# Performance work log

Hardware: AMD Instinct MI355X
Metric: run time of the kernel (lower is better)

Reference implementation:

```python
import jax, jax.numpy as jnp
import numpy as np

N_EMBD = 4096
N_HEAD = 2
HEAD_DIM = N_EMBD // N_HEAD  # 2048; note seq_len T must equal HEAD_DIM for the bias broadcast
B, T = 8, HEAD_DIM


def setup_inputs() -> dict:
    key = jax.random.key(0)
    ks = jax.random.split(key, 6)
    s = 1.0 / np.sqrt(N_EMBD)
    return {
        "x": jax.random.normal(ks[0], (B, T, N_EMBD), dtype=jnp.float32),
        "Wq": jax.random.normal(ks[1], (N_EMBD, N_EMBD), dtype=jnp.float32) * s,
        "Wk": jax.random.normal(ks[2], (N_EMBD, N_EMBD), dtype=jnp.float32) * s,
        "Wv": jax.random.normal(ks[3], (N_EMBD, N_EMBD), dtype=jnp.float32) * s,
        "Wo": jax.random.normal(ks[4], (N_EMBD, N_EMBD), dtype=jnp.float32) * s,
        "position_bias": jax.random.normal(ks[5], (N_HEAD, HEAD_DIM), dtype=jnp.float32) * 0.02,
    }


def reference(x, Wq, Wk, Wv, Wo, position_bias):
    Bb, Tt, C = x.shape
    H, D = N_HEAD, C // N_HEAD
    # nn.Linear(bias=False): y = x @ W.T
    q = (x @ Wq.T).reshape(Bb, Tt, H, D).transpose(0, 2, 1, 3)  # (B,H,T,D)
    k = (x @ Wk.T).reshape(Bb, Tt, H, D).transpose(0, 2, 1, 3)
    v = (x @ Wv.T).reshape(Bb, Tt, H, D).transpose(0, 2, 1, 3)
    scale = 1.0 / jnp.sqrt(jnp.asarray(D, dtype=x.dtype))
    scores = jnp.einsum("bhtd,bhsd->bhts", q, k) * scale  # (B,H,T,T)
    # position_bias (H,D) -> (1,H,1,D); broadcasts over key axis since D == T
    scores = scores + position_bias[None, :, None, :]
    atten = jax.nn.softmax(scores, axis=-1)  # mask=None, dropout=0.0 -> identity
    y = jnp.einsum("bhts,bhsd->bhtd", atten, v)  # (B,H,T,D)
    y = y.transpose(0, 2, 1, 3).reshape(Bb, Tt, C)
    y = y @ Wo.T
    return (y, atten)
```

## Files before the change

### kernel.cpp

```cpp
#include <hip/hip_runtime.h>
#include <hip/hip_bf16.h>
#include <cstdint>
#include <cstddef>


typedef short short8_t __attribute__((ext_vector_type(8)));
typedef float f32x4   __attribute__((ext_vector_type(4)));

__device__ __forceinline__ short f2bf(float f) {
  unsigned u = __builtin_bit_cast(unsigned, f);
  u = (u + 0x7FFFu + ((u >> 16) & 1u)) >> 16;
  return (short)u;
}

__device__ __forceinline__ short8_t cvt8(float4 a, float4 b) {
  short8_t r;
  r[0] = f2bf(a.x); r[1] = f2bf(a.y); r[2] = f2bf(a.z); r[3] = f2bf(a.w);
  r[4] = f2bf(b.x); r[5] = f2bf(b.y); r[6] = f2bf(b.z); r[7] = f2bf(b.w);
  return r;
}

__device__ __forceinline__ void gld_lds16(const void* g, void* l) {
  __builtin_amdgcn_global_load_lds(
      (const __attribute__((address_space(1))) void*)g,
      (__attribute__((address_space(3))) void*)l, 16, 0, 0);
}

__global__ __launch_bounds__(256)
void cvt_f32_bf16(const float* __restrict__ src, short* __restrict__ dst, int n8) {
  for (int i = blockIdx.x * blockDim.x + threadIdx.x; i < n8;
       i += gridDim.x * blockDim.x) {
    const float4* p = (const float4*)(src + (size_t)i * 8);
    float4 a = p[0], b = p[1];
    *(short8_t*)(dst + (size_t)i * 8) = cvt8(a, b);
  }
}

template<int MODE>
__global__ __launch_bounds__(512, 2)
void gemm256(const short* __restrict__ Ag, const short* __restrict__ Bg,
             void* __restrict__ Cg, const float* __restrict__ bias) {
  constexpr int K  = (MODE == 3 || MODE == 4) ? 2048 : 4096;
  constexpr int NS = K / 32;

  __shared__ short lds[65536];

  const int tid = threadIdx.x;

  const int bid = blockIdx.x;
  const int id  = (bid & 7) * (gridDim.x >> 3) + (bid >> 3);

  int m0, n0, z = 0;
  size_t aoff = 0, boff = 0;
  if constexpr (MODE == 3 || MODE == 4) {
    z  = id >> 6;
    m0 = ((id >> 3) & 7) << 8;
    n0 = (id & 7) << 8;
    aoff = boff = (size_t)z << 22;
  } else {
    m0 = (id >> 4) << 8;
    n0 = (id & 15) << 8;
  }

  const int r0 = tid >> 2;
  const int qs = ((tid & 3) ^ ((r0 >> 1) & 3)) << 3;
  const short* Ap0 = Ag + aoff + (size_t)(m0 + r0) * K + qs;
  const short* Ap1 = Ap0 + (size_t)128 * K;
  const short* Bp0 = Bg + boff + (size_t)(n0 + r0) * K + qs;
  const short* Bp1 = Bp0 + (size_t)128 * K;
  short* la0 = &lds[0]    + tid * 8;
  short* la1 = la0 + 4096;
  short* lb0 = &lds[8192] + tid * 8;
  short* lb1 = lb0 + 4096;

  auto STAGE = [&](int t) {
    const int s = (t & 3) * 16384;
    const int k = t * 32;
    gld_lds16(Ap0 + k, la0 + s);
    gld_lds16(Ap1 + k, la1 + s);
    gld_lds16(Bp0 + k, lb0 + s);
    gld_lds16(Bp1 + k, lb1 + s);
  };

  const int l  = tid & 63;
  const int fr = l & 15;
  const int kq = l >> 4;
  const int wm = (tid >> 8) << 7;
  const int wn = ((tid >> 6) & 3) << 6;
  const int slotP = (kq ^ ((fr >> 1) & 3)) << 3;
  const int aB = (wm + fr) * 32 + slotP;
  const int bB = 8192 + (wn + fr) * 32 + slotP;

  f32x4 acc[8][4] = {};

  STAGE(0); STAGE(1); STAGE(2);

  for (int p = 0; p < NS; ++p) {
    if (p + 3 < NS) {
      STAGE(p + 3);
      asm volatile("s_waitcnt vmcnt(12)" ::: "memory");
    } else if (p + 2 < NS) {
      asm volatile("s_waitcnt vmcnt(8)" ::: "memory");
    } else if (p + 1 < NS) {
      asm volatile("s_waitcnt vmcnt(4)" ::: "memory");
    } else {
      asm volatile("s_waitcnt vmcnt(0)" ::: "memory");
    }
    __builtin_amdgcn_s_barrier();
    __builtin_amdgcn_sched_barrier(0);

    const short* sl = &lds[(p & 3) * 16384];
    short8_t af[8], bf[4];
#pragma unroll
    for (int m = 0; m < 8; ++m) af[m] = *(const short8_t*)&sl[aB + m * 512];
#pragma unroll
    for (int n = 0; n < 4; ++n) bf[n] = *(const short8_t*)&sl[bB + n * 512];
    __builtin_amdgcn_s_setprio(1);
#pragma unroll
    for (int m = 0; m < 8; ++m)
#pragma unroll
      for (int n = 0; n < 4; ++n)
        acc[m][n] = __builtin_amdgcn_mfma_f32_16x16x32_bf16(af[m], bf[n], acc[m][n], 0, 0, 0);
    __builtin_amdgcn_s_setprio(0);
    __builtin_amdgcn_sched_barrier(0);
    __builtin_amdgcn_s_barrier();
  }

#pragma unroll
  for (int m = 0; m < 8; ++m) {
#pragma unroll
    for (int n = 0; n < 4; ++n) {
#pragma unroll
      for (int r = 0; r < 4; ++r) {
        const int gm = m0 + wm + m * 16 + kq * 4 + r;
        const int gn = n0 + wn + n * 16 + fr;
        const float v = acc[m][n][r];
        if constexpr (MODE == 0) {
          short* dst = (short*)Cg;
          const int bh = ((gm >> 11) << 1) + (gn >> 11);
          dst[((size_t)bh << 22) + ((size_t)(gm & 2047) << 11) + (gn & 2047)] = f2bf(v);
        } else if constexpr (MODE == 2) {
          short* dst = (short*)Cg;
          const int bh = ((gm >> 11) << 1) + (gn >> 11);
          dst[((size_t)bh << 22) + ((size_t)(gn & 2047) << 11) + (gm & 2047)] = f2bf(v);
        } else if constexpr (MODE == 3) {
          float* dst = (float*)Cg;
          const float sv = v * 0.022097086912079608f + bias[((z & 1) << 11) + gn];
          dst[((size_t)z << 22) + ((size_t)gm << 11) + gn] = sv;
        } else if constexpr (MODE == 4) {
          short* dst = (short*)Cg;
          const size_t row = ((size_t)(z >> 1) << 11) + gm;
          dst[(row << 12) + ((size_t)(z & 1) << 11) + gn] = f2bf(v);
        } else {
          float* dst = (float*)Cg;
          dst[(size_t)gm * 4096 + gn] = v;
        }
      }
    }
  }
}

__global__ __launch_bounds__(256)
void softmax_rows(float* __restrict__ attn, short* __restrict__ outb) {
  float* row  = attn + ((size_t)blockIdx.x << 11);
  short* rowb = outb + ((size_t)blockIdx.x << 11);
  const int tid = threadIdx.x;

  float4 v0 = *(const float4*)(row + tid * 8);
  float4 v1 = *(const float4*)(row + tid * 8 + 4);

  float m = fmaxf(fmaxf(fmaxf(v0.x, v0.y), fmaxf(v0.z, v0.w)),
                  fmaxf(fmaxf(v1.x, v1.y), fmaxf(v1.z, v1.w)));
#pragma unroll
  for (int off = 1; off < 64; off <<= 1) m = fmaxf(m, __shfl_xor(m, off));

  __shared__ float redm[4];
  __shared__ float reds[4];
  if ((tid & 63) == 0) redm[tid >> 6] = m;
  __syncthreads();
  m = fmaxf(fmaxf(redm[0], redm[1]), fmaxf(redm[2], redm[3]));

  float e[8];
  e[0] = expf(v0.x - m); e[1] = expf(v0.y - m); e[2] = expf(v0.z - m); e[3] = expf(v0.w - m);
  e[4] = expf(v1.x - m); e[5] = expf(v1.y - m); e[6] = expf(v1.z - m); e[7] = expf(v1.w - m);
  float s = 0.f;
#pragma unroll
  for (int i = 0; i < 8; ++i) s += e[i];
#pragma unroll
  for (int off = 1; off < 64; off <<= 1) s += __shfl_xor(s, off);
  if ((tid & 63) == 0) reds[tid >> 6] = s;
  __syncthreads();
  s = reds[0] + reds[1] + reds[2] + reds[3];

  const float inv = 1.0f / s;
  float4 o0, o1;
  o0.x = e[0] * inv; o0.y = e[1] * inv; o0.z = e[2] * inv; o0.w = e[3] * inv;
  o1.x = e[4] * inv; o1.y = e[5] * inv; o1.z = e[6] * inv; o1.w = e[7] * inv;
  *(float4*)(row + tid * 8)     = o0;
  *(float4*)(row + tid * 8 + 4) = o1;
  *(short8_t*)(rowb + tid * 8)  = cvt8(o0, o1);
}

extern "C" void kernel_launch(void* const* d_in, const int* in_sizes, int n_in,
                              void* d_out, int out_size, void* d_ws, size_t ws_size,
                              hipStream_t stream) {
  const float* x  = (const float*)d_in[0];
  const float* Wq = (const float*)d_in[1];
  const float* Wk = (const float*)d_in[2];
  const float* Wv = (const float*)d_in[3];
  const float* Wo = (const float*)d_in[4];
  const float* pb = (const float*)d_in[5];

  float* y_out = (float*)d_out;
  float* attn  = y_out + (size_t)8 * 2048 * 4096;

  const size_t NEED = 4ull * 67108864ull * 2ull;
  if (ws_size < NEED) return;
  short* buf0 = (short*)d_ws;
  short* buf1 = buf0 + 67108864;
  short* buf2 = buf1 + 67108864;
  short* buf3 = buf2 + 67108864;

  short* xb      = buf0;
  short* qb      = buf1;
  short* kb      = buf2;
  short* vtb     = buf3;
  short* wob     = buf0;
  short* attn_bf = buf1;
  short* yb      = buf2;
  short* wb      = (short*)attn;

  const dim3 blk512(512);
  const dim3 blk(256);
  const dim3 gcv(2048);
  const dim3 g1k(1024);

  cvt_f32_bf16<<<gcv, blk, 0, stream>>>(x, xb, 67108864 / 8);

  cvt_f32_bf16<<<gcv, blk, 0, stream>>>(Wq, wb, 16777216 / 8);
  gemm256<0><<<g1k, blk512, 0, stream>>>(xb, wb, qb, nullptr);
  cvt_f32_bf16<<<gcv, blk, 0, stream>>>(Wk, wb, 16777216 / 8);
  gemm256<0><<<g1k, blk512, 0, stream>>>(xb, wb, kb, nullptr);
  cvt_f32_bf16<<<gcv, blk, 0, stream>>>(Wv, wb, 16777216 / 8);
  gemm256<2><<<g1k, blk512, 0, stream>>>(xb, wb, vtb, nullptr);

  cvt_f32_bf16<<<gcv, blk, 0, stream>>>(Wo, wob, 16777216 / 8);

  gemm256<3><<<g1k, blk512, 0, stream>>>(qb, kb, attn, pb);
  softmax_rows<<<dim3(32768), blk, 0, stream>>>(attn, attn_bf);
  gemm256<4><<<g1k, blk512, 0, stream>>>(attn_bf, vtb, yb, nullptr);
  gemm256<5><<<g1k, blk512, 0, stream>>>(yb, wob, y_out, nullptr);
}
```

Measured before the change: 3.011 ms.

## Double-buffer MFMA register fragments to prefetch next LDS stage during compute

Restructures the GEMM main loop so that the fragments for stage p+1 are read from LDS into a second register set while the MFMAs for stage p run, using a ping-pong pair of fragment arrays and a two-phase unrolled loop. Wait counts shift by one stage, and the sched_barriers that kept the LDS reads separate from the MFMA block are removed so the compiler can interleave them. The goal is to hide LDS read latency behind matrix math. In exchange it holds twelve more short8 fragments in registers, which raises register pressure under the 512-thread, 2-block launch bound and risks spills.

```diff
diff --git a/kernel.cpp b/kernel.cpp
--- a/kernel.cpp
+++ b/kernel.cpp
@@ -92,38 +92,50 @@
   const int bB = 8192 + (wn + fr) * 32 + slotP;
 
   f32x4 acc[8][4] = {};
-
-  STAGE(0); STAGE(1); STAGE(2);
-
-  for (int p = 0; p < NS; ++p) {
+  short8_t fA[8], fB[4], gA[8], gB[4];
+
+  auto phase = [&](int p, short8_t (&cA)[8], short8_t (&cB)[4],
+                   short8_t (&nA)[8], short8_t (&nB)[4]) {
     if (p + 3 < NS) {
       STAGE(p + 3);
-      asm volatile("s_waitcnt vmcnt(12)" ::: "memory");
+      asm volatile("s_waitcnt vmcnt(8)" ::: "memory");
     } else if (p + 2 < NS) {
-      asm volatile("s_waitcnt vmcnt(8)" ::: "memory");
+      asm volatile("s_waitcnt vmcnt(4)" ::: "memory");
     } else if (p + 1 < NS) {
-      asm volatile("s_waitcnt vmcnt(4)" ::: "memory");
-    } else {
       asm volatile("s_waitcnt vmcnt(0)" ::: "memory");
     }
     __builtin_amdgcn_s_barrier();
-    __builtin_amdgcn_sched_barrier(0);
-
-    const short* sl = &lds[(p & 3) * 16384];
-    short8_t af[8], bf[4];
-#pragma unroll
-    for (int m = 0; m < 8; ++m) af[m] = *(const short8_t*)&sl[aB + m * 512];
-#pragma unroll
-    for (int n = 0; n < 4; ++n) bf[n] = *(const short8_t*)&sl[bB + n * 512];
+    if (p + 1 < NS) {
+      const short* sl = &lds[((p + 1) & 3) * 16384];
+#pragma unroll
+      for (int m = 0; m < 8; ++m) nA[m] = *(const short8_t*)&sl[aB + m * 512];
+#pragma unroll
+      for (int n = 0; n < 4; ++n) nB[n] = *(const short8_t*)&sl[bB + n * 512];
+    }
     __builtin_amdgcn_s_setprio(1);
 #pragma unroll
     for (int m = 0; m < 8; ++m)
 #pragma unroll
       for (int n = 0; n < 4; ++n)
-        acc[m][n] = __builtin_amdgcn_mfma_f32_16x16x32_bf16(af[m], bf[n], acc[m][n], 0, 0, 0);
+        acc[m][n] = __builtin_amdgcn_mfma_f32_16x16x32_bf16(cA[m], cB[n], acc[m][n], 0, 0, 0);
     __builtin_amdgcn_s_setprio(0);
-    __builtin_amdgcn_sched_barrier(0);
     __builtin_amdgcn_s_barrier();
+  };
+
+  STAGE(0); STAGE(1); STAGE(2);
+  asm volatile("s_waitcnt vmcnt(8)" ::: "memory");
+  __builtin_amdgcn_s_barrier();
+  {
+    const short* sl = &lds[0];
+#pragma unroll
+    for (int m = 0; m < 8; ++m) fA[m] = *(const short8_t*)&sl[aB + m * 512];
+#pragma unroll
+    for (int n = 0; n < 4; ++n) fB[n] = *(const short8_t*)&sl[bB + n * 512];
+  }
+
+  for (int p = 0; p < NS; p += 2) {
+    phase(p,     fA, fB, gA, gB);
+    phase(p + 1, gA, gB, fA, fB);
   }
 
 #pragma unroll
```

Result: faster. 2.925 ms (-2.9%).

## Split GEMM k-step into two half-phases with fragment-ordered LDS layout

Applied to the files above, without the earlier changes.

Reworks the GEMM mainloop so each 32-wide k-step runs in two halves. Each half issues half of the next stage's global-to-LDS loads and loads A fragments for half of the M tiles, with barriers between halves so memory traffic interleaves with MFMA work. The LDS tile layout changes from a swizzled row-major layout to a per-16-row fragment-contiguous layout, so each lane reads one contiguous 16-byte chunk without XOR swizzling. This adds barriers per iteration and changes the vmcnt accounting, which risks extra sync stalls or ordering mistakes.

```diff
diff --git a/kernel.cpp b/kernel.cpp
--- a/kernel.cpp
+++ b/kernel.cpp
@@ -62,70 +62,94 @@
     n0 = (id & 15) << 8;
   }
 
-  const int r0 = tid >> 2;
-  const int qs = ((tid & 3) ^ ((r0 >> 1) & 3)) << 3;
-  const short* Ap0 = Ag + aoff + (size_t)(m0 + r0) * K + qs;
-  const short* Ap1 = Ap0 + (size_t)128 * K;
-  const short* Bp0 = Bg + boff + (size_t)(n0 + r0) * K + qs;
-  const short* Bp1 = Bp0 + (size_t)128 * K;
-  short* la0 = &lds[0]    + tid * 8;
-  short* la1 = la0 + 4096;
-  short* lb0 = &lds[8192] + tid * 8;
-  short* lb1 = lb0 + 4096;
-
-  auto STAGE = [&](int t) {
-    const int s = (t & 3) * 16384;
+  const int l = tid & 63;
+  const int w = tid >> 6;
+
+  const int srow = l & 15;
+  const int skol = (l >> 4) * 8;
+  const short* ApS  = Ag + aoff + (size_t)(m0 + 2 * w * 16 + srow) * K + skol;
+  const short* ApS2 = ApS + (size_t)16 * K;
+  const short* BpS  = Bg + boff + (size_t)(n0 + 2 * w * 16 + srow) * K + skol;
+  const short* BpS2 = BpS + (size_t)16 * K;
+
+  auto STAGE0 = [&](int t) {
+    const int s = (t & 3) << 14;
     const int k = t * 32;
-    gld_lds16(Ap0 + k, la0 + s);
-    gld_lds16(Ap1 + k, la1 + s);
-    gld_lds16(Bp0 + k, lb0 + s);
-    gld_lds16(Bp1 + k, lb1 + s);
+    gld_lds16(ApS + k, &lds[s + 2 * w * 512]);
+    gld_lds16(BpS + k, &lds[s + 8192 + 2 * w * 512]);
   };
-
-  const int l  = tid & 63;
+  auto STAGE1 = [&](int t) {
+    const int s = (t & 3) << 14;
+    const int k = t * 32;
+    gld_lds16(ApS2 + k, &lds[s + (2 * w + 1) * 512]);
+    gld_lds16(BpS2 + k, &lds[s + 8192 + (2 * w + 1) * 512]);
+  };
+
+  const int wmF = (tid >> 8) * 8;
+  const int wnF = ((tid >> 6) & 3) * 4;
+  const int l8  = l * 8;
+
+  f32x4 acc[8][4] = {};
+
+  STAGE0(0); STAGE1(0); STAGE0(1); STAGE1(1); STAGE0(2); STAGE1(2);
+  asm volatile("s_waitcnt vmcnt(8)" ::: "memory");
+  __builtin_amdgcn_s_barrier();
+
+  for (int p = 0; p < NS; ++p) {
+    const int slot = (p & 3) << 14;
+    short8_t A4[4], B4[4], A8[4];
+
+#pragma unroll
+    for (int n = 0; n < 4; ++n)
+      B4[n] = *(const short8_t*)&lds[slot + 8192 + (wnF + n) * 512 + l8];
+#pragma unroll
+    for (int i = 0; i < 4; ++i)
+      A4[i] = *(const short8_t*)&lds[slot + (wmF + i) * 512 + l8];
+    if (p + 3 < NS) STAGE0(p + 3);
+    __builtin_amdgcn_sched_barrier(0);
+    __builtin_amdgcn_s_barrier();
+    asm volatile("s_waitcnt lgkmcnt(0)" ::: "memory");
+    __builtin_amdgcn_sched_barrier(0);
+    __builtin_amdgcn_s_setprio(1);
+#pragma unroll
+    for (int i = 0; i < 4; ++i)
+#pragma unroll
+      for (int n = 0; n < 4; ++n)
+        acc[i][n] = __builtin_amdgcn_mfma_f32_16x16x32_bf16(A4[i], B4[n], acc[i][n], 0, 0, 0);
+    __builtin_amdgcn_s_setprio(0);
+    __builtin_amdgcn_sched_barrier(0);
+    __builtin_amdgcn_s_barrier();
+
+#pragma unroll
+    for (int i = 0; i < 4; ++i)
+      A8[i] = *(const short8_t*)&lds[slot + (wmF + 4 + i) * 512 + l8];
+    if (p + 3 < NS) {
+      STAGE1(p + 3);
+      asm volatile("s_waitcnt vmcnt(8)" ::: "memory");
+    } else if (p + 2 < NS) {
+      asm volatile("s_waitcnt vmcnt(4)" ::: "memory");
+    } else if (p + 1 < NS) {
+      asm volatile("s_waitcnt vmcnt(0)" ::: "memory");
+    }
+    __builtin_amdgcn_sched_barrier(0);
+    __builtin_amdgcn_s_barrier();
+    asm volatile("s_waitcnt lgkmcnt(0)" ::: "memory");
+    __builtin_amdgcn_sched_barrier(0);
+    __builtin_amdgcn_s_setprio(1);
+#pragma unroll
+    for (int i = 0; i < 4; ++i)
+#pragma unroll
+      for (int n = 0; n < 4; ++n)
+        acc[4 + i][n] = __builtin_amdgcn_mfma_f32_16x16x32_bf16(A8[i], B4[n], acc[4 + i][n], 0, 0, 0);
+    __builtin_amdgcn_s_setprio(0);
+    __builtin_amdgcn_sched_barrier(0);
+    __builtin_amdgcn_s_barrier();
+  }
+
   const int fr = l & 15;
   const int kq = l >> 4;
   const int wm = (tid >> 8) << 7;
   const int wn = ((tid >> 6) & 3) << 6;
-  const int slotP = (kq ^ ((fr >> 1) & 3)) << 3;
-  const int aB = (wm + fr) * 32 + slotP;
-  const int bB = 8192 + (wn + fr) * 32 + slotP;
-
-  f32x4 acc[8][4] = {};
-
-  STAGE(0); STAGE(1); STAGE(2);
-
-  for (int p = 0; p < NS; ++p) {
-    if (p + 3 < NS) {
-      STAGE(p + 3);
-      asm volatile("s_waitcnt vmcnt(12)" ::: "memory");
-    } else if (p + 2 < NS) {
-      asm volatile("s_waitcnt vmcnt(8)" ::: "memory");
-    } else if (p + 1 < NS) {
-      asm volatile("s_waitcnt vmcnt(4)" ::: "memory");
-    } else {
-      asm volatile("s_waitcnt vmcnt(0)" ::: "memory");
-    }
-    __builtin_amdgcn_s_barrier();
-    __builtin_amdgcn_sched_barrier(0);
-
-    const short* sl = &lds[(p & 3) * 16384];
-    short8_t af[8], bf[4];
-#pragma unroll
-    for (int m = 0; m < 8; ++m) af[m] = *(const short8_t*)&sl[aB + m * 512];
-#pragma unroll
-    for (int n = 0; n < 4; ++n) bf[n] = *(const short8_t*)&sl[bB + n * 512];
-    __builtin_amdgcn_s_setprio(1);
-#pragma unroll
-    for (int m = 0; m < 8; ++m)
-#pragma unroll
-      for (int n = 0; n < 4; ++n)
-        acc[m][n] = __builtin_amdgcn_mfma_f32_16x16x32_bf16(af[m], bf[n], acc[m][n], 0, 0, 0);
-    __builtin_amdgcn_s_setprio(0);
-    __builtin_amdgcn_sched_barrier(0);
-    __builtin_amdgcn_s_barrier();
-  }
-
 #pragma unroll
   for (int m = 0; m < 8; ++m) {
 #pragma unroll
```

New measurement: 3.219 ms. 6.9% more time.

## Fuse QKV projections into one GEMM and switch to 32x32x16 MFMA tiles

Applied to the files above, without the earlier changes.

Concatenates the bf16 Wq/Wk/Wv into one weight buffer and runs a single 3072-block GEMM whose epilogue routes columns to the q, k or transposed-v outputs. The GEMM core moves from 16x16x32 to 32x32x16 bf16 MFMAs with a new unswizzled LDS staging layout. It also drops the trailing barrier by issuing the next stage after the top barrier. The goal is fewer launches, better wave occupancy on the projection, and fewer LDS reads per MFMA. The unswizzled LDS layout may cause bank conflicts, and removing the second barrier relies on the 4-slot ring buffer to avoid overwriting data still being read.

```diff
diff --git a/kernel.cpp b/kernel.cpp
--- a/kernel.cpp
+++ b/kernel.cpp
@@ -5,7 +5,7 @@
 
 
 typedef short short8_t __attribute__((ext_vector_type(8)));
-typedef float f32x4   __attribute__((ext_vector_type(4)));
+typedef float f32x16  __attribute__((ext_vector_type(16)));
 
 __device__ __forceinline__ short f2bf(float f) {
   unsigned u = __builtin_bit_cast(unsigned, f);
@@ -39,7 +39,8 @@
 template<int MODE>
 __global__ __launch_bounds__(512, 2)
 void gemm256(const short* __restrict__ Ag, const short* __restrict__ Bg,
-             void* __restrict__ Cg, const float* __restrict__ bias) {
+             void* __restrict__ Cg, void* __restrict__ C2, void* __restrict__ C3,
+             const float* __restrict__ bias) {
   constexpr int K  = (MODE == 3 || MODE == 4) ? 2048 : 4096;
   constexpr int NS = K / 32;
 
@@ -57,100 +58,107 @@
     m0 = ((id >> 3) & 7) << 8;
     n0 = (id & 7) << 8;
     aoff = boff = (size_t)z << 22;
+  } else if constexpr (MODE == 0) {
+    m0 = (id / 48) << 8;
+    n0 = (id % 48) << 8;
   } else {
     m0 = (id >> 4) << 8;
     n0 = (id & 15) << 8;
   }
 
-  const int r0 = tid >> 2;
-  const int qs = ((tid & 3) ^ ((r0 >> 1) & 3)) << 3;
-  const short* Ap0 = Ag + aoff + (size_t)(m0 + r0) * K + qs;
-  const short* Ap1 = Ap0 + (size_t)128 * K;
-  const short* Bp0 = Bg + boff + (size_t)(n0 + r0) * K + qs;
-  const short* Bp1 = Bp0 + (size_t)128 * K;
-  short* la0 = &lds[0]    + tid * 8;
-  short* la1 = la0 + 4096;
-  short* lb0 = &lds[8192] + tid * 8;
-  short* lb1 = lb0 + 4096;
+  const int l = tid & 63;
+  const int w = tid >> 6;
+
+  const int srow = l & 31;
+  const int sk8  = (l >> 5) * 8;
+  const short* ApS0 = Ag + aoff + (size_t)(m0 + w * 32 + srow) * K + sk8;
+  const short* ApS1 = ApS0 + 16;
+  const short* BpS0 = Bg + boff + (size_t)(n0 + w * 32 + srow) * K + sk8;
+  const short* BpS1 = BpS0 + 16;
+  short* lA0 = &lds[(2 * w + 0) * 512 + l * 8];
+  short* lA1 = &lds[(2 * w + 1) * 512 + l * 8];
+  short* lB0 = &lds[8192 + (2 * w + 0) * 512 + l * 8];
+  short* lB1 = &lds[8192 + (2 * w + 1) * 512 + l * 8];
 
   auto STAGE = [&](int t) {
-    const int s = (t & 3) * 16384;
+    const int s = (t & 3) << 14;
     const int k = t * 32;
-    gld_lds16(Ap0 + k, la0 + s);
-    gld_lds16(Ap1 + k, la1 + s);
-    gld_lds16(Bp0 + k, lb0 + s);
-    gld_lds16(Bp1 + k, lb1 + s);
+    gld_lds16(ApS0 + k, lA0 + s);
+    gld_lds16(ApS1 + k, lA1 + s);
+    gld_lds16(BpS0 + k, lB0 + s);
+    gld_lds16(BpS1 + k, lB1 + s);
   };
 
-  const int l  = tid & 63;
-  const int fr = l & 15;
-  const int kq = l >> 4;
-  const int wm = (tid >> 8) << 7;
-  const int wn = ((tid >> 6) & 3) << 6;
-  const int slotP = (kq ^ ((fr >> 1) & 3)) << 3;
-  const int aB = (wm + fr) * 32 + slotP;
-  const int bB = 8192 + (wn + fr) * 32 + slotP;
-
-  f32x4 acc[8][4] = {};
+  const int wmF = (w >> 2) * 4;
+  const int wnF = (w & 3) * 2;
+  const int l8  = l * 8;
+
+  f32x16 acc[4][2] = {};
 
   STAGE(0); STAGE(1); STAGE(2);
 
   for (int p = 0; p < NS; ++p) {
-    if (p + 3 < NS) {
-      STAGE(p + 3);
-      asm volatile("s_waitcnt vmcnt(12)" ::: "memory");
-    } else if (p + 2 < NS) {
-      asm volatile("s_waitcnt vmcnt(8)" ::: "memory");
-    } else if (p + 1 < NS) {
-      asm volatile("s_waitcnt vmcnt(4)" ::: "memory");
-    } else {
-      asm volatile("s_waitcnt vmcnt(0)" ::: "memory");
-    }
+    if (p + 2 < NS)      asm volatile("s_waitcnt vmcnt(8)" ::: "memory");
+    else if (p + 1 < NS) asm volatile("s_waitcnt vmcnt(4)" ::: "memory");
+    else                 asm volatile("s_waitcnt vmcnt(0)" ::: "memory");
     __builtin_amdgcn_s_barrier();
-    __builtin_amdgcn_sched_barrier(0);
-
-    const short* sl = &lds[(p & 3) * 16384];
-    short8_t af[8], bf[4];
-#pragma unroll
-    for (int m = 0; m < 8; ++m) af[m] = *(const short8_t*)&sl[aB + m * 512];
-#pragma unroll
-    for (int n = 0; n < 4; ++n) bf[n] = *(const short8_t*)&sl[bB + n * 512];
+
+    if (p + 3 < NS) STAGE(p + 3);
+
+    const int slot = (p & 3) << 14;
+    short8_t A[4][2], B[2][2];
+#pragma unroll
+    for (int i = 0; i < 4; ++i)
+#pragma unroll
+      for (int kh = 0; kh < 2; ++kh)
+        A[i][kh] = *(const short8_t*)&lds[slot + ((wmF + i) * 2 + kh) * 512 + l8];
+#pragma unroll
+    for (int j = 0; j < 2; ++j)
+#pragma unroll
+      for (int kh = 0; kh < 2; ++kh)
+        B[j][kh] = *(const short8_t*)&lds[slot + 8192 + ((wnF + j) * 2 + kh) * 512 + l8];
+
     __builtin_amdgcn_s_setprio(1);
 #pragma unroll
-    for (int m = 0; m < 8; ++m)
-#pragma unroll
-      for (int n = 0; n < 4; ++n)
-        acc[m][n] = __builtin_amdgcn_mfma_f32_16x16x32_bf16(af[m], bf[n], acc[m][n], 0, 0, 0);
+    for (int kh = 0; kh < 2; ++kh)
+#pragma unroll
+      for (int i = 0; i < 4; ++i)
+#pragma unroll
+        for (int j = 0; j < 2; ++j)
+          acc[i][j] = __builtin_amdgcn_mfma_f32_32x32x16_bf16(A[i][kh], B[j][kh], acc[i][j], 0, 0, 0);
     __builtin_amdgcn_s_setprio(0);
-    __builtin_amdgcn_sched_barrier(0);
-    __builtin_amdgcn_s_barrier();
-  }
-
-#pragma unroll
-  for (int m = 0; m < 8; ++m) {
-#pragma unroll
-    for (int n = 0; n < 4; ++n) {
-#pragma unroll
-      for (int r = 0; r < 4; ++r) {
-        const int gm = m0 + wm + m * 16 + kq * 4 + r;
-        const int gn = n0 + wn + n * 16 + fr;
-        const float v = acc[m][n][r];
+  }
+
+  const int col = l & 31;
+  const int rhi = (l >> 5) * 4;
+#pragma unroll
+  for (int i = 0; i < 4; ++i) {
+#pragma unroll
+    for (int j = 0; j < 2; ++j) {
+#pragma unroll
+      for (int r = 0; r < 16; ++r) {
+        const int row = (r & 3) + 8 * (r >> 2) + rhi;
+        const int gm  = m0 + (w >> 2) * 128 + i * 32 + row;
+        const int gn  = n0 + (w & 3) * 64 + j * 32 + col;
+        const float v = acc[i][j][r];
         if constexpr (MODE == 0) {
-          short* dst = (short*)Cg;
-          const int bh = ((gm >> 11) << 1) + (gn >> 11);
-          dst[((size_t)bh << 22) + ((size_t)(gm & 2047) << 11) + (gn & 2047)] = f2bf(v);
-        } else if constexpr (MODE == 2) {
-          short* dst = (short*)Cg;
-          const int bh = ((gm >> 11) << 1) + (gn >> 11);
-          dst[((size_t)bh << 22) + ((size_t)(gn & 2047) << 11) + (gm & 2047)] = f2bf(v);
+          const int wsel = gn >> 12;
+          const int c    = gn & 4095;
+          const int bh   = ((gm >> 11) << 1) + (c >> 11);
+          if (wsel == 2) {
+            ((short*)C3)[((size_t)bh << 22) + ((size_t)(c & 2047) << 11) + (gm & 2047)] = f2bf(v);
+          } else {
+            short* dst = wsel ? (short*)C2 : (short*)Cg;
+            dst[((size_t)bh << 22) + ((size_t)(gm & 2047) << 11) + (c & 2047)] = f2bf(v);
+          }
         } else if constexpr (MODE == 3) {
           float* dst = (float*)Cg;
           const float sv = v * 0.022097086912079608f + bias[((z & 1) << 11) + gn];
           dst[((size_t)z << 22) + ((size_t)gm << 11) + gn] = sv;
         } else if constexpr (MODE == 4) {
           short* dst = (short*)Cg;
-          const size_t row = ((size_t)(z >> 1) << 11) + gm;
-          dst[(row << 12) + ((size_t)(z & 1) << 11) + gn] = f2bf(v);
+          const size_t orow = ((size_t)(z >> 1) << 11) + gm;
+          dst[(orow << 12) + ((size_t)(z & 1) << 11) + gn] = f2bf(v);
         } else {
           float* dst = (float*)Cg;
           dst[(size_t)gm * 4096 + gn] = v;
@@ -228,26 +236,23 @@
   short* wob     = buf0;
   short* attn_bf = buf1;
   short* yb      = buf2;
-  short* wb      = (short*)attn;
+  short* wqkv    = (short*)attn;
 
   const dim3 blk512(512);
   const dim3 blk(256);
   const dim3 gcv(2048);
-  const dim3 g1k(1024);
 
   cvt_f32_bf16<<<gcv, blk, 0, stream>>>(x, xb, 67108864 / 8);
-
-  cvt_f32_bf16<<<gcv, blk, 0, stream>>>(Wq, wb, 16777216 / 8);
-  gemm256<0><<<g1k, blk512, 0, stream>>>(xb, wb, qb, nullptr);
-  cvt_f32_bf16<<<gcv, blk, 0, stream>>>(Wk, wb, 16777216 / 8);
-  gemm256<0><<<g1k, blk512, 0, stream>>>(xb, wb, kb, nullptr);
-  cvt_f32_bf16<<<gcv, blk, 0, stream>>>(Wv, wb, 16777216 / 8);
-  gemm256<2><<<g1k, blk512, 0, stream>>>(xb, wb, vtb, nullptr);
+  cvt_f32_bf16<<<gcv, blk, 0, stream>>>(Wq, wqkv,                 16777216 / 8);
+  cvt_f32_bf16<<<gcv, blk, 0, stream>>>(Wk, wqkv + 16777216,      16777216 / 8);
+  cvt_f32_bf16<<<gcv, blk, 0, stream>>>(Wv, wqkv + 2 * 16777216,  16777216 / 8);
+
+  gemm256<0><<<dim3(3072), blk512, 0, stream>>>(xb, wqkv, qb, kb, vtb, nullptr);
 
   cvt_f32_bf16<<<gcv, blk, 0, stream>>>(Wo, wob, 16777216 / 8);
 
-  gemm256<3><<<g1k, blk512, 0, stream>>>(qb, kb, attn, pb);
+  gemm256<3><<<dim3(1024), blk512, 0, stream>>>(qb, kb, attn, nullptr, nullptr, pb);
   softmax_rows<<<dim3(32768), blk, 0, stream>>>(attn, attn_bf);
-  gemm256<4><<<g1k, blk512, 0, stream>>>(attn_bf, vtb, yb, nullptr);
-  gemm256<5><<<g1k, blk512, 0, stream>>>(yb, wob, y_out, nullptr);
-}
+  gemm256<4><<<dim3(1024), blk512, 0, stream>>>(attn_bf, vtb, yb, nullptr, nullptr, nullptr);
+  gemm256<5><<<dim3(1024), blk512, 0, stream>>>(yb, wob, y_out, nullptr, nullptr, nullptr);
+}
```

Result: slower. 3.664 ms (+21.7%).
